# Kernel optimization log

Measured on AMD Instinct MI355X. Metric: run time of the kernel, lower is better.

## Reference

```python
import jax, jax.numpy as jnp
import numpy as np

INPUT_SIZE = 128
HID = 64
B, T = 256, 1024

def setup_inputs() -> dict:
    key = jax.random.key(0)
    ks = jax.random.split(key, 12)
    s1 = 1.0 / np.sqrt(HID)
    def u(k, shape):
        return jax.random.uniform(k, shape, jnp.float32, -s1, s1)
    return {
        "x": jax.random.normal(ks[0], (B, T, INPUT_SIZE), jnp.float32),
        "w_ih0": u(ks[1], (4 * HID, INPUT_SIZE)),
        "w_hh0": u(ks[2], (4 * HID, HID)),
        "b_ih0": u(ks[3], (4 * HID,)),
        "b_hh0": u(ks[4], (4 * HID,)),
        "w_ih1": u(ks[5], (4 * HID, HID)),
        "w_hh1": u(ks[6], (4 * HID, HID)),
        "b_ih1": u(ks[7], (4 * HID,)),
        "b_hh1": u(ks[8], (4 * HID,)),
        "w_out": u(ks[9], (1, HID)),
        "b_out": u(ks[10], (1,)),
    }

def _lstm(x, w_ih, w_hh, b_ih, b_hh):
    # x: [B, T, I] -> h sequence [B, T, H]; PyTorch gate order i, f, g, o
    Bb = x.shape[0]
    H = w_hh.shape[1]
    # precompute input contribution for all timesteps (one big GEMM)
    xg = jnp.einsum('bti,gi->btg', x, w_ih) + b_ih + b_hh  # [B, T, 4H]
    def step(carry, g_t):
        h, c = carry
        g = g_t + h @ w_hh.T  # [B, 4H]
        i, f, gg, o = jnp.split(g, 4, axis=-1)
        i = jax.nn.sigmoid(i)
        f = jax.nn.sigmoid(f)
        gg = jnp.tanh(gg)
        o = jax.nn.sigmoid(o)
        c = f * c + i * gg
        h = o * jnp.tanh(c)
        return (h, c), h
    init = (jnp.zeros((Bb, H), x.dtype), jnp.zeros((Bb, H), x.dtype))
    _, hs = jax.lax.scan(step, init, jnp.swapaxes(xg, 0, 1))  # [T, B, H]
    return jnp.swapaxes(hs, 0, 1)

def reference(x, w_ih0, w_hh0, b_ih0, b_hh0, w_ih1, w_hh1, b_ih1, b_hh1, w_out, b_out):
    h1 = _lstm(x, w_ih0, w_hh0, b_ih0, b_hh0)   # [B, T, H]
    h2 = _lstm(h1, w_ih1, w_hh1, b_ih1, b_hh1)  # [B, T, H]
    logits = jnp.einsum('bth,oh->bto', h2, w_out) + b_out  # [B, T, 1]
    return jax.nn.sigmoid(logits)
```

## Files before the change

### kernel.cpp

```cpp
#include <hip/hip_runtime.h>

#define BB 256
#define TT 1024
#define II 128
#define HH 64
#define BT (BB * TT)

typedef _Float16 h2 __attribute__((ext_vector_type(2)));
typedef _Float16 half8 __attribute__((ext_vector_type(8)));
typedef float f32x4 __attribute__((ext_vector_type(4)));
typedef unsigned int uint;
typedef unsigned short ushort;

#define DOT2(a, b, c) __builtin_amdgcn_fdot2((a), (b), (c), false)
#define BC(u) __builtin_bit_cast(h2, (uint)(u))
#define MFMA16(a, b, c) __builtin_amdgcn_mfma_f32_16x16x32_f16((a), (b), (c), 0, 0, 0)
#define SIG(v) __builtin_amdgcn_rcpf(1.0f + __expf(-(v)))
#define TNH(v) (1.0f - 2.0f * __builtin_amdgcn_rcpf(1.0f + __expf(2.0f * (v))))

#define BAR() asm volatile("s_waitcnt lgkmcnt(0)\n\ts_barrier" ::: "memory")

#define LDPK(P, ptr) uint P; { float2 _f = *(const float2*)(ptr); \
    h2 _h; _h[0] = (_Float16)_f.x; _h[1] = (_Float16)_f.y; \
    P = __builtin_bit_cast(uint, _h); }
#define PIN8(a,b,c,d,e,f,g,h_) asm volatile("" : "+v"(a),"+v"(b),"+v"(c),"+v"(d),"+v"(e),"+v"(f),"+v"(g),"+v"(h_));
#define LD8(P, base, o) \
    LDPK(P##0,(base)+(o)+ 0) LDPK(P##1,(base)+(o)+ 2) LDPK(P##2,(base)+(o)+ 4) LDPK(P##3,(base)+(o)+ 6) \
    LDPK(P##4,(base)+(o)+ 8) LDPK(P##5,(base)+(o)+10) LDPK(P##6,(base)+(o)+12) LDPK(P##7,(base)+(o)+14) \
    PIN8(P##0,P##1,P##2,P##3,P##4,P##5,P##6,P##7)

#define D8A(P, va, vb, c0, c1, c2, c3) \
    c0 = DOT2(BC(P##0), BC((va).x), c0); c1 = DOT2(BC(P##1), BC((va).y), c1); \
    c2 = DOT2(BC(P##2), BC((va).z), c2); c3 = DOT2(BC(P##3), BC((va).w), c3); \
    c0 = DOT2(BC(P##4), BC((vb).x), c0); c1 = DOT2(BC(P##5), BC((vb).y), c1); \
    c2 = DOT2(BC(P##6), BC((vb).z), c2); c3 = DOT2(BC(P##7), BC((vb).w), c3);

#define GDOT(G, s) { float a0=0.f,a1=0.f,a2=0.f,a3=0.f; \
    D8A(G##A, hv0, hv1, a0,a1,a2,a3) D8A(G##B, hv2, hv3, a0,a1,a2,a3) \
    D8A(G##C, hv4, hv5, a0,a1,a2,a3) D8A(G##D, hv6, hv7, a0,a1,a2,a3) \
    s = (a0 + a1) + (a2 + a3); }

__global__ __launch_bounds__(256)
void xg_mfma(const float* __restrict__ x, const float* __restrict__ w_ih0,
             ushort* __restrict__ xg)
{
    __shared__ __align__(16) _Float16 xt[64][136];
    __shared__ __align__(16) _Float16 wt[128][136];
    const int tid = threadIdx.x, lane = tid & 63, wv = tid >> 6;
    const int bt0 = blockIdx.x * 64;
    {
        const int row = tid >> 2, q = (tid & 3) * 32;
        const float4* src = (const float4*)(x + (size_t)(bt0 + row) * II + q);
        _Float16* dst = &xt[row][q];
        #pragma unroll
        for (int i = 0; i < 8; ++i) {
            float4 v = src[i];
            dst[4*i+0]=(_Float16)v.x; dst[4*i+1]=(_Float16)v.y;
            dst[4*i+2]=(_Float16)v.z; dst[4*i+3]=(_Float16)v.w;
        }
    }
    for (int nh = 0; nh < 2; ++nh) {
        __syncthreads();
        {
            const int n = tid >> 1, kh = (tid & 1) * 64;
            const float4* src = (const float4*)(w_ih0 + (size_t)(nh * 128 + n) * II + kh);
            _Float16* dst = &wt[n][kh];
            #pragma unroll
            for (int i = 0; i < 16; ++i) {
                float4 v = src[i];
                dst[4*i+0]=(_Float16)v.x; dst[4*i+1]=(_Float16)v.y;
                dst[4*i+2]=(_Float16)v.z; dst[4*i+3]=(_Float16)v.w;
            }
        }
        __syncthreads();
        const int m = wv * 16 + (lane & 15);
        const int kf = (lane >> 4) * 8;
        half8 a0 = *(const half8*)&xt[m][ 0 + kf];
        half8 a1 = *(const half8*)&xt[m][32 + kf];
        half8 a2 = *(const half8*)&xt[m][64 + kf];
        half8 a3 = *(const half8*)&xt[m][96 + kf];
        #pragma unroll
        for (int nt = 0; nt < 8; ++nt) {
            const int nloc = nt * 16 + (lane & 15);
            half8 b0 = *(const half8*)&wt[nloc][ 0 + kf];
            half8 b1 = *(const half8*)&wt[nloc][32 + kf];
            half8 b2 = *(const half8*)&wt[nloc][64 + kf];
            half8 b3 = *(const half8*)&wt[nloc][96 + kf];
            f32x4 acc = {0.f, 0.f, 0.f, 0.f};
            acc = MFMA16(a0, b0, acc); acc = MFMA16(a1, b1, acc);
            acc = MFMA16(a2, b2, acc); acc = MFMA16(a3, b3, acc);
            const int col = nh * 128 + nt * 16 + (lane & 15);
            const int idx = (col & 63) * 4 + (col >> 6);
            const int r0  = wv * 16 + (lane >> 4) * 4;
            #pragma unroll
            for (int r = 0; r < 4; ++r) {
                _Float16 hv = (_Float16)acc[r];
                xg[(size_t)(bt0 + r0 + r) * 256 + idx] = __builtin_bit_cast(ushort, hv);
            }
        }
    }
}

__global__ __launch_bounds__(192) __attribute__((amdgpu_waves_per_eu(1, 1)))
void lstm2_core(const float* __restrict__ w_hh0,
                const float* __restrict__ b_ih0, const float* __restrict__ b_hh0,
                const float* __restrict__ w_ih1, const float* __restrict__ w_hh1,
                const float* __restrict__ b_ih1, const float* __restrict__ b_hh1,
                const ushort* __restrict__ xg, ushort* __restrict__ h1g)
{
    const int bb = blockIdx.x;
    const int w  = threadIdx.x >> 6;
    const int j  = threadIdx.x & 63;

    __shared__ __align__(16) uint  h0buf[2][32];
    __shared__ __align__(16) uint  h1buf[2][32];
    __shared__ float zbuf[2][4][68];

    const float* Wsel = (w == 0) ? w_hh0 : (w == 1) ? w_ih1 : w_hh1;
    const float* r0p = Wsel + (size_t)(  0 + j) * 64;
    const float* r1p = Wsel + (size_t)( 64 + j) * 64;
    const float* r2p = Wsel + (size_t)(128 + j) * 64;
    const float* r3p = Wsel + (size_t)(192 + j) * 64;
    LD8(G0A, r0p,  0) LD8(G0B, r0p, 16) LD8(G0C, r0p, 32) LD8(G0D, r0p, 48)
    LD8(G1A, r1p,  0) LD8(G1B, r1p, 16) LD8(G1C, r1p, 32) LD8(G1D, r1p, 48)
    LD8(G2A, r2p,  0) LD8(G2B, r2p, 16) LD8(G2C, r2p, 32) LD8(G2D, r2p, 48)
    LD8(G3A, r3p,  0) LD8(G3B, r3p, 16) LD8(G3C, r3p, 32) LD8(G3D, r3p, 48)

    float bI = 0.f, bF = 0.f, bG = 0.f, bO = 0.f;
    if (w == 0) {
        bI = b_ih0[j]       + b_hh0[j];
        bF = b_ih0[64 + j]  + b_hh0[64 + j];
        bG = b_ih0[128 + j] + b_hh0[128 + j];
        bO = b_ih0[192 + j] + b_hh0[192 + j];
    } else if (w == 2) {
        bI = b_ih1[j]       + b_hh1[j];
        bF = b_ih1[64 + j]  + b_hh1[64 + j];
        bG = b_ih1[128 + j] + b_hh1[128 + j];
        bO = b_ih1[192 + j] + b_hh1[192 + j];
    }

    float cst = 0.0f;
    const ushort* xbase = xg + (size_t)bb * TT * 256 + j * 4;
    ushort* h1b = h1g + (size_t)bb * TT * 64 + j;

    if (threadIdx.x < 32)       h0buf[1][threadIdx.x] = 0u;
    else if (threadIdx.x < 64)  h1buf[1][threadIdx.x - 32] = 0u;
    __syncthreads();

    uint2 xc = {0,0}, xn1 = {0,0}, xn2 = {0,0};
    if (w == 0) {
        xc  = *(const uint2*)(xbase);
        xn1 = *(const uint2*)(xbase + 256);
    }

    for (int k = 0; k < TT + 2; ++k) {
        if (w == 0) {
            if (k + 2 < TT) xn2 = *(const uint2*)(xbase + (size_t)(k + 2) * 256);
            if (k < TT) {
                const uint4* hq = (const uint4*)&h0buf[(k + 1) & 1][0];
                uint4 hv0=hq[0], hv1=hq[1], hv2=hq[2], hv3=hq[3];
                uint4 hv4=hq[4], hv5=hq[5], hv6=hq[6], hv7=hq[7];
                float si, sf, sg, so;
                GDOT(G0, si) GDOT(G1, sf) GDOT(G2, sg) GDOT(G3, so)
                h2 xlo = BC(xc.x), xhi = BC(xc.y);
                si += bI + (float)xlo[0]; sf += bF + (float)xlo[1];
                sg += bG + (float)xhi[0]; so += bO + (float)xhi[1];
                float ii = SIG(si), ff = SIG(sf), gg = TNH(sg), oo = SIG(so);
                cst = fmaf(ff, cst, ii * gg);
                float hval = oo * TNH(cst);
                ((_Float16*)&h0buf[k & 1][0])[j] = (_Float16)hval;
            }
            xc = xn1; xn1 = xn2;
        } else if (w == 1) {
            if (k >= 1 && k <= TT) {
                const int m = k - 1;
                const uint4* hq = (const uint4*)&h0buf[m & 1][0];
                uint4 hv0=hq[0], hv1=hq[1], hv2=hq[2], hv3=hq[3];
                uint4 hv4=hq[4], hv5=hq[5], hv6=hq[6], hv7=hq[7];
                float si, sf, sg, so;
                GDOT(G0, si) GDOT(G1, sf) GDOT(G2, sg) GDOT(G3, so)
                const int s = m & 1;
                zbuf[s][0][j] = si; zbuf[s][1][j] = sf;
                zbuf[s][2][j] = sg; zbuf[s][3][j] = so;
            }
        } else {
            if (k >= 2) {
                const int m = k - 2;
                const int s = m & 1;
                const uint4* hq = (const uint4*)&h1buf[(m + 1) & 1][0];
                uint4 hv0=hq[0], hv1=hq[1], hv2=hq[2], hv3=hq[3];
                uint4 hv4=hq[4], hv5=hq[5], hv6=hq[6], hv7=hq[7];
                float si, sf, sg, so;
                GDOT(G0, si) GDOT(G1, sf) GDOT(G2, sg) GDOT(G3, so)
                si += bI + zbuf[s][0][j]; sf += bF + zbuf[s][1][j];
                sg += bG + zbuf[s][2][j]; so += bO + zbuf[s][3][j];
                float ii = SIG(si), ff = SIG(sf), gg = TNH(sg), oo = SIG(so);
                cst = fmaf(ff, cst, ii * gg);
                float hval = oo * TNH(cst);
                _Float16 hf = (_Float16)hval;
                ((_Float16*)&h1buf[m & 1][0])[j] = hf;
                h1b[(size_t)m * 64] = __builtin_bit_cast(ushort, hf);
            }
        }
        BAR();
    }
}

__global__ __launch_bounds__(256)
void head_gemv(const ushort* __restrict__ h1g, const float* __restrict__ w_out,
               const float* __restrict__ b_out, float* __restrict__ outp)
{
    __shared__ float wsh[64];
    const int tid = threadIdx.x;
    if (tid < 64) wsh[tid] = w_out[tid];
    __syncthreads();
    const int bt = blockIdx.x * 256 + tid;
    const uint4* hp = (const uint4*)(h1g + (size_t)bt * 64);
    float s = 0.0f;
    #pragma unroll
    for (int i = 0; i < 8; ++i) {
        uint4 v = hp[i];
        const float* wp = &wsh[8 * i];
        h2 p;
        p = BC(v.x); s = fmaf((float)p[0], wp[0], s); s = fmaf((float)p[1], wp[1], s);
        p = BC(v.y); s = fmaf((float)p[0], wp[2], s); s = fmaf((float)p[1], wp[3], s);
        p = BC(v.z); s = fmaf((float)p[0], wp[4], s); s = fmaf((float)p[1], wp[5], s);
        p = BC(v.w); s = fmaf((float)p[0], wp[6], s); s = fmaf((float)p[1], wp[7], s);
    }
    outp[bt] = __builtin_amdgcn_rcpf(1.0f + __expf(-(s + b_out[0])));
}

extern "C" void kernel_launch(void* const* d_in, const int* in_sizes, int n_in,
                              void* d_out, int out_size, void* d_ws, size_t ws_size,
                              hipStream_t stream) {
    const float* x     = (const float*)d_in[0];
    const float* w_ih0 = (const float*)d_in[1];
    const float* w_hh0 = (const float*)d_in[2];
    const float* b_ih0 = (const float*)d_in[3];
    const float* b_hh0 = (const float*)d_in[4];
    const float* w_ih1 = (const float*)d_in[5];
    const float* w_hh1 = (const float*)d_in[6];
    const float* b_ih1 = (const float*)d_in[7];
    const float* b_hh1 = (const float*)d_in[8];
    const float* w_out = (const float*)d_in[9];
    const float* b_out = (const float*)d_in[10];
    float* out = (float*)d_out;

    ushort* xg  = (ushort*)d_ws;
    ushort* h1g = (ushort*)((char*)d_ws + (size_t)BT * 256 * 2);

    hipLaunchKernelGGL(xg_mfma, dim3(BT / 64), dim3(256), 0, stream, x, w_ih0, xg);
    hipLaunchKernelGGL(lstm2_core, dim3(BB), dim3(192), 0, stream,
                       w_hh0, b_ih0, b_hh0, w_ih1, w_hh1, b_ih1, b_hh1, xg, h1g);
    hipLaunchKernelGGL(head_gemv, dim3(BT / 256), dim3(256), 0, stream,
                       h1g, w_out, b_out, out);
}
```

Baseline: 823.1 us.

## Split LSTM gate rows across two waves per role to halve serial dot chain

The recurrent kernel now uses six waves instead of three: each role (layer-0 recurrence, layer-1 input projection, layer-1 recurrence) is split over two waves, and each lane computes two gate rows instead of four. Gate activations are exchanged between lane halves with cross-lane shuffles. The xg layout is changed to plain gate-major columns to match. This shortens the per-timestep dependent dot-product chain at the cost of extra shuffles, scalar 16-bit global loads, and a six-wave barrier each step.

```diff
diff --git a/kernel.cpp b/kernel.cpp
--- a/kernel.cpp
+++ b/kernel.cpp
@@ -15,8 +15,7 @@
 #define DOT2(a, b, c) __builtin_amdgcn_fdot2((a), (b), (c), false)
 #define BC(u) __builtin_bit_cast(h2, (uint)(u))
 #define MFMA16(a, b, c) __builtin_amdgcn_mfma_f32_16x16x32_f16((a), (b), (c), 0, 0, 0)
-#define SIG(v) __builtin_amdgcn_rcpf(1.0f + __expf(-(v)))
-#define TNH(v) (1.0f - 2.0f * __builtin_amdgcn_rcpf(1.0f + __expf(2.0f * (v))))
+#define RCP(v) __builtin_amdgcn_rcpf(v)
 
 #define BAR() asm volatile("s_waitcnt lgkmcnt(0)\n\ts_barrier" ::: "memory")
 
@@ -35,10 +34,13 @@
     c0 = DOT2(BC(P##4), BC((vb).x), c0); c1 = DOT2(BC(P##5), BC((vb).y), c1); \
     c2 = DOT2(BC(P##6), BC((vb).z), c2); c3 = DOT2(BC(P##7), BC((vb).w), c3);
 
-#define GDOT(G, s) { float a0=0.f,a1=0.f,a2=0.f,a3=0.f; \
-    D8A(G##A, hv0, hv1, a0,a1,a2,a3) D8A(G##B, hv2, hv3, a0,a1,a2,a3) \
-    D8A(G##C, hv4, hv5, a0,a1,a2,a3) D8A(G##D, hv6, hv7, a0,a1,a2,a3) \
-    s = (a0 + a1) + (a2 + a3); }
+#define DUALDOT(sA, sB) { \
+    float a0=0.f,a1=0.f,a2=0.f,a3=0.f, b0=0.f,b1=0.f,b2=0.f,b3=0.f; \
+    D8A(A0, hv0, hv1, a0,a1,a2,a3) D8A(A1, hv2, hv3, a0,a1,a2,a3) \
+    D8A(A2, hv4, hv5, a0,a1,a2,a3) D8A(A3, hv6, hv7, a0,a1,a2,a3) \
+    D8A(B0, hv0, hv1, b0,b1,b2,b3) D8A(B1, hv2, hv3, b0,b1,b2,b3) \
+    D8A(B2, hv4, hv5, b0,b1,b2,b3) D8A(B3, hv6, hv7, b0,b1,b2,b3) \
+    sA = (a0 + a1) + (a2 + a3); sB = (b0 + b1) + (b2 + b3); }
 
 __global__ __launch_bounds__(256)
 void xg_mfma(const float* __restrict__ x, const float* __restrict__ w_ih0,
@@ -90,116 +92,128 @@
             acc = MFMA16(a0, b0, acc); acc = MFMA16(a1, b1, acc);
             acc = MFMA16(a2, b2, acc); acc = MFMA16(a3, b3, acc);
             const int col = nh * 128 + nt * 16 + (lane & 15);
-            const int idx = (col & 63) * 4 + (col >> 6);
             const int r0  = wv * 16 + (lane >> 4) * 4;
             #pragma unroll
             for (int r = 0; r < 4; ++r) {
                 _Float16 hv = (_Float16)acc[r];
-                xg[(size_t)(bt0 + r0 + r) * 256 + idx] = __builtin_bit_cast(ushort, hv);
-            }
-        }
-    }
-}
-
-__global__ __launch_bounds__(192) __attribute__((amdgpu_waves_per_eu(1, 1)))
+                xg[(size_t)(bt0 + r0 + r) * 256 + col] = __builtin_bit_cast(ushort, hv);
+            }
+        }
+    }
+}
+
+__global__ __launch_bounds__(384) __attribute__((amdgpu_waves_per_eu(1, 1)))
 void lstm2_core(const float* __restrict__ w_hh0,
                 const float* __restrict__ b_ih0, const float* __restrict__ b_hh0,
                 const float* __restrict__ w_ih1, const float* __restrict__ w_hh1,
                 const float* __restrict__ b_ih1, const float* __restrict__ b_hh1,
                 const ushort* __restrict__ xg, ushort* __restrict__ h1g)
 {
-    const int bb = blockIdx.x;
-    const int w  = threadIdx.x >> 6;
-    const int j  = threadIdx.x & 63;
-
-    __shared__ __align__(16) uint  h0buf[2][32];
-    __shared__ __align__(16) uint  h1buf[2][32];
+    const int bb   = blockIdx.x;
+    const int w    = threadIdx.x >> 6;
+    const int l    = threadIdx.x & 63;
+    const int role = w >> 1;
+    const int gp   = l >> 5;
+    const int j    = (w & 1) * 32 + (l & 31);
+    const int rA   = gp * 128 + j;
+    const int rB   = rA + 64;
+
+    __shared__ __align__(16) uint h0buf[2][32];
+    __shared__ __align__(16) uint h1buf[2][32];
     __shared__ float zbuf[2][4][68];
 
-    const float* Wsel = (w == 0) ? w_hh0 : (w == 1) ? w_ih1 : w_hh1;
-    const float* r0p = Wsel + (size_t)(  0 + j) * 64;
-    const float* r1p = Wsel + (size_t)( 64 + j) * 64;
-    const float* r2p = Wsel + (size_t)(128 + j) * 64;
-    const float* r3p = Wsel + (size_t)(192 + j) * 64;
-    LD8(G0A, r0p,  0) LD8(G0B, r0p, 16) LD8(G0C, r0p, 32) LD8(G0D, r0p, 48)
-    LD8(G1A, r1p,  0) LD8(G1B, r1p, 16) LD8(G1C, r1p, 32) LD8(G1D, r1p, 48)
-    LD8(G2A, r2p,  0) LD8(G2B, r2p, 16) LD8(G2C, r2p, 32) LD8(G2D, r2p, 48)
-    LD8(G3A, r3p,  0) LD8(G3B, r3p, 16) LD8(G3C, r3p, 32) LD8(G3D, r3p, 48)
-
-    float bI = 0.f, bF = 0.f, bG = 0.f, bO = 0.f;
-    if (w == 0) {
-        bI = b_ih0[j]       + b_hh0[j];
-        bF = b_ih0[64 + j]  + b_hh0[64 + j];
-        bG = b_ih0[128 + j] + b_hh0[128 + j];
-        bO = b_ih0[192 + j] + b_hh0[192 + j];
-    } else if (w == 2) {
-        bI = b_ih1[j]       + b_hh1[j];
-        bF = b_ih1[64 + j]  + b_hh1[64 + j];
-        bG = b_ih1[128 + j] + b_hh1[128 + j];
-        bO = b_ih1[192 + j] + b_hh1[192 + j];
-    }
+    const float* M = (role == 0) ? w_hh0 : (role == 1) ? w_ih1 : w_hh1;
+    const float* pA = M + (size_t)rA * 64;
+    const float* pB = M + (size_t)rB * 64;
+    LD8(A0, pA,  0) LD8(A1, pA, 16) LD8(A2, pA, 32) LD8(A3, pA, 48)
+    LD8(B0, pB,  0) LD8(B1, pB, 16) LD8(B2, pB, 32) LD8(B3, pB, 48)
+
+    float bA = 0.f, bB = 0.f;
+    if (role == 0)      { bA = b_ih0[rA] + b_hh0[rA]; bB = b_ih0[rB] + b_hh0[rB]; }
+    else if (role == 1) { bA = b_ih1[rA] + b_hh1[rA]; bB = b_ih1[rB] + b_hh1[rB]; }
+
+    const float nscA = gp ?  2.0f : -1.0f;
+    const float acoA = gp ?  1.0f :  0.0f;
+    const float bcoA = gp ? -1.0f :  1.0f;
 
     float cst = 0.0f;
-    const ushort* xbase = xg + (size_t)bb * TT * 256 + j * 4;
+    const ushort* xbA = xg + (size_t)bb * TT * 256 + rA;
+    const ushort* xbB = xg + (size_t)bb * TT * 256 + rB;
     ushort* h1b = h1g + (size_t)bb * TT * 64 + j;
 
-    if (threadIdx.x < 32)       h0buf[1][threadIdx.x] = 0u;
-    else if (threadIdx.x < 64)  h1buf[1][threadIdx.x - 32] = 0u;
+    if (threadIdx.x < 32)      h0buf[1][threadIdx.x] = 0u;
+    else if (threadIdx.x < 64) h1buf[1][threadIdx.x - 32] = 0u;
     __syncthreads();
 
-    uint2 xc = {0,0}, xn1 = {0,0}, xn2 = {0,0};
-    if (w == 0) {
-        xc  = *(const uint2*)(xbase);
-        xn1 = *(const uint2*)(xbase + 256);
+    ushort xcA = 0, xcB = 0, x1A = 0, x1B = 0, x2A = 0, x2B = 0;
+    if (role == 0) {
+        xcA = xbA[0];   xcB = xbB[0];
+        x1A = xbA[256]; x1B = xbB[256];
     }
 
     for (int k = 0; k < TT + 2; ++k) {
-        if (w == 0) {
-            if (k + 2 < TT) xn2 = *(const uint2*)(xbase + (size_t)(k + 2) * 256);
+        if (role == 0) {
+            if (k + 2 < TT) { x2A = xbA[(size_t)(k + 2) * 256];
+                              x2B = xbB[(size_t)(k + 2) * 256]; }
             if (k < TT) {
                 const uint4* hq = (const uint4*)&h0buf[(k + 1) & 1][0];
                 uint4 hv0=hq[0], hv1=hq[1], hv2=hq[2], hv3=hq[3];
                 uint4 hv4=hq[4], hv5=hq[5], hv6=hq[6], hv7=hq[7];
-                float si, sf, sg, so;
-                GDOT(G0, si) GDOT(G1, sf) GDOT(G2, sg) GDOT(G3, so)
-                h2 xlo = BC(xc.x), xhi = BC(xc.y);
-                si += bI + (float)xlo[0]; sf += bF + (float)xlo[1];
-                sg += bG + (float)xhi[0]; so += bO + (float)xhi[1];
-                float ii = SIG(si), ff = SIG(sf), gg = TNH(sg), oo = SIG(so);
+                float sA, sB;
+                DUALDOT(sA, sB)
+                sA += bA + (float)__builtin_bit_cast(_Float16, xcA);
+                sB += bB + (float)__builtin_bit_cast(_Float16, xcB);
+                float yA   = __expf(nscA * sA);
+                float actA = fmaf(acoA, yA, bcoA) * RCP(yA + 1.0f);
+                float actB = RCP(1.0f + __expf(-sB));
+                float oA = __shfl_xor(actA, 32, 64);
+                float oB = __shfl_xor(actB, 32, 64);
+                float ii = gp ? oA : actA;
+                float ff = gp ? oB : actB;
+                float gg = gp ? actA : oA;
+                float oo = gp ? actB : oB;
                 cst = fmaf(ff, cst, ii * gg);
-                float hval = oo * TNH(cst);
-                ((_Float16*)&h0buf[k & 1][0])[j] = (_Float16)hval;
-            }
-            xc = xn1; xn1 = xn2;
-        } else if (w == 1) {
+                float hval = oo * (1.0f - 2.0f * RCP(1.0f + __expf(2.0f * cst)));
+                if (gp == 0) ((_Float16*)&h0buf[k & 1][0])[j] = (_Float16)hval;
+            }
+            xcA = x1A; xcB = x1B; x1A = x2A; x1B = x2B;
+        } else if (role == 1) {
             if (k >= 1 && k <= TT) {
-                const int m = k - 1;
-                const uint4* hq = (const uint4*)&h0buf[m & 1][0];
+                const int m = k - 1, s = m & 1;
+                const uint4* hq = (const uint4*)&h0buf[s][0];
                 uint4 hv0=hq[0], hv1=hq[1], hv2=hq[2], hv3=hq[3];
                 uint4 hv4=hq[4], hv5=hq[5], hv6=hq[6], hv7=hq[7];
-                float si, sf, sg, so;
-                GDOT(G0, si) GDOT(G1, sf) GDOT(G2, sg) GDOT(G3, so)
-                const int s = m & 1;
-                zbuf[s][0][j] = si; zbuf[s][1][j] = sf;
-                zbuf[s][2][j] = sg; zbuf[s][3][j] = so;
+                float sA, sB;
+                DUALDOT(sA, sB)
+                zbuf[s][2 * gp][j]     = sA + bA;
+                zbuf[s][2 * gp + 1][j] = sB + bB;
             }
         } else {
             if (k >= 2) {
-                const int m = k - 2;
-                const int s = m & 1;
+                const int m = k - 2, s = m & 1;
                 const uint4* hq = (const uint4*)&h1buf[(m + 1) & 1][0];
                 uint4 hv0=hq[0], hv1=hq[1], hv2=hq[2], hv3=hq[3];
                 uint4 hv4=hq[4], hv5=hq[5], hv6=hq[6], hv7=hq[7];
-                float si, sf, sg, so;
-                GDOT(G0, si) GDOT(G1, sf) GDOT(G2, sg) GDOT(G3, so)
-                si += bI + zbuf[s][0][j]; sf += bF + zbuf[s][1][j];
-                sg += bG + zbuf[s][2][j]; so += bO + zbuf[s][3][j];
-                float ii = SIG(si), ff = SIG(sf), gg = TNH(sg), oo = SIG(so);
+                float sA, sB;
+                DUALDOT(sA, sB)
+                sA += zbuf[s][2 * gp][j];
+                sB += zbuf[s][2 * gp + 1][j];
+                float yA   = __expf(nscA * sA);
+                float actA = fmaf(acoA, yA, bcoA) * RCP(yA + 1.0f);
+                float actB = RCP(1.0f + __expf(-sB));
+                float oA = __shfl_xor(actA, 32, 64);
+                float oB = __shfl_xor(actB, 32, 64);
+                float ii = gp ? oA : actA;
+                float ff = gp ? oB : actB;
+                float gg = gp ? actA : oA;
+                float oo = gp ? actB : oB;
                 cst = fmaf(ff, cst, ii * gg);
-                float hval = oo * TNH(cst);
-                _Float16 hf = (_Float16)hval;
-                ((_Float16*)&h1buf[m & 1][0])[j] = hf;
-                h1b[(size_t)m * 64] = __builtin_bit_cast(ushort, hf);
+                float hval = oo * (1.0f - 2.0f * RCP(1.0f + __expf(2.0f * cst)));
+                if (gp == 0) {
+                    _Float16 hf = (_Float16)hval;
+                    ((_Float16*)&h1buf[s][0])[j] = hf;
+                    h1b[(size_t)m * 64] = __builtin_bit_cast(ushort, hf);
+                }
             }
         }
         BAR();
@@ -227,7 +241,7 @@
         p = BC(v.z); s = fmaf((float)p[0], wp[4], s); s = fmaf((float)p[1], wp[5], s);
         p = BC(v.w); s = fmaf((float)p[0], wp[6], s); s = fmaf((float)p[1], wp[7], s);
     }
-    outp[bt] = __builtin_amdgcn_rcpf(1.0f + __expf(-(s + b_out[0])));
+    outp[bt] = RCP(1.0f + __expf(-(s + b_out[0])));
 }
 
 extern "C" void kernel_launch(void* const* d_in, const int* in_sizes, int n_in,
@@ -250,7 +264,7 @@
     ushort* h1g = (ushort*)((char*)d_ws + (size_t)BT * 256 * 2);
 
     hipLaunchKernelGGL(xg_mfma, dim3(BT / 64), dim3(256), 0, stream, x, w_ih0, xg);
-    hipLaunchKernelGGL(lstm2_core, dim3(BB), dim3(192), 0, stream,
+    hipLaunchKernelGGL(lstm2_core, dim3(BB), dim3(384), 0, stream,
                        w_hh0, b_ih0, b_hh0, w_ih1, w_hh1, b_ih1, b_hh1, xg, h1g);
     hipLaunchKernelGGL(head_gemv, dim3(BT / 256), dim3(256), 0, stream,
                        h1g, w_out, b_out, out);
```

Measured after the change: 884.7 us. +7.5%, slower.

## Keep full W_ih0 resident per block and unroll recurrence loop by two

Applied to the files above, without the earlier changes.

The input-projection kernel now loads all 256 rows of w_ih0 into shared memory once and loops over four 64-row x tiles, so each block covers 256 timesteps and the weight reload and conversion are amortised. The recurrent kernel is manually unrolled by two with compile-time buffer parity, replacing the three-deep x prefetch rotation with two alternating registers. This removes per-step index arithmetic and register moves on the serial critical path. The trade-off is larger shared memory per projection block and fewer blocks for the projection.

```diff
diff --git a/kernel.cpp b/kernel.cpp
--- a/kernel.cpp
+++ b/kernel.cpp
@@ -44,43 +44,47 @@
 void xg_mfma(const float* __restrict__ x, const float* __restrict__ w_ih0,
              ushort* __restrict__ xg)
 {
+    __shared__ __align__(16) _Float16 wt[256][136];
     __shared__ __align__(16) _Float16 xt[64][136];
-    __shared__ __align__(16) _Float16 wt[128][136];
     const int tid = threadIdx.x, lane = tid & 63, wv = tid >> 6;
-    const int bt0 = blockIdx.x * 64;
-    {
-        const int row = tid >> 2, q = (tid & 3) * 32;
-        const float4* src = (const float4*)(x + (size_t)(bt0 + row) * II + q);
-        _Float16* dst = &xt[row][q];
+    const int bt0 = blockIdx.x * 256;
+
+    #pragma unroll
+    for (int p = 0; p < 2; ++p) {
+        const int n = p * 128 + (tid >> 1), kh = (tid & 1) * 64;
+        const float4* src = (const float4*)(w_ih0 + (size_t)n * II + kh);
+        _Float16* dst = &wt[n][kh];
         #pragma unroll
-        for (int i = 0; i < 8; ++i) {
+        for (int i = 0; i < 16; ++i) {
             float4 v = src[i];
             dst[4*i+0]=(_Float16)v.x; dst[4*i+1]=(_Float16)v.y;
             dst[4*i+2]=(_Float16)v.z; dst[4*i+3]=(_Float16)v.w;
         }
     }
-    for (int nh = 0; nh < 2; ++nh) {
+
+    for (int grp = 0; grp < 4; ++grp) {
         __syncthreads();
         {
-            const int n = tid >> 1, kh = (tid & 1) * 64;
-            const float4* src = (const float4*)(w_ih0 + (size_t)(nh * 128 + n) * II + kh);
-            _Float16* dst = &wt[n][kh];
+            const int row = tid >> 2, q = (tid & 3) * 32;
+            const float4* src = (const float4*)(x + (size_t)(bt0 + grp * 64 + row) * II + q);
+            _Float16* dst = &xt[row][q];
             #pragma unroll
-            for (int i = 0; i < 16; ++i) {
+            for (int i = 0; i < 8; ++i) {
                 float4 v = src[i];
                 dst[4*i+0]=(_Float16)v.x; dst[4*i+1]=(_Float16)v.y;
                 dst[4*i+2]=(_Float16)v.z; dst[4*i+3]=(_Float16)v.w;
             }
         }
         __syncthreads();
-        const int m = wv * 16 + (lane & 15);
+
+        const int m  = wv * 16 + (lane & 15);
         const int kf = (lane >> 4) * 8;
         half8 a0 = *(const half8*)&xt[m][ 0 + kf];
         half8 a1 = *(const half8*)&xt[m][32 + kf];
         half8 a2 = *(const half8*)&xt[m][64 + kf];
         half8 a3 = *(const half8*)&xt[m][96 + kf];
         #pragma unroll
-        for (int nt = 0; nt < 8; ++nt) {
+        for (int nt = 0; nt < 16; ++nt) {
             const int nloc = nt * 16 + (lane & 15);
             half8 b0 = *(const half8*)&wt[nloc][ 0 + kf];
             half8 b1 = *(const half8*)&wt[nloc][32 + kf];
@@ -89,9 +93,9 @@
             f32x4 acc = {0.f, 0.f, 0.f, 0.f};
             acc = MFMA16(a0, b0, acc); acc = MFMA16(a1, b1, acc);
             acc = MFMA16(a2, b2, acc); acc = MFMA16(a3, b3, acc);
-            const int col = nh * 128 + nt * 16 + (lane & 15);
+            const int col = nt * 16 + (lane & 15);
             const int idx = (col & 63) * 4 + (col >> 6);
-            const int r0  = wv * 16 + (lane >> 4) * 4;
+            const int r0  = grp * 64 + wv * 16 + (lane >> 4) * 4;
             #pragma unroll
             for (int r = 0; r < 4; ++r) {
                 _Float16 hv = (_Float16)acc[r];
@@ -100,6 +104,50 @@
         }
     }
 }
+
+#define STEP(K_, E_, XC_) { \
+    if (w == 0) { \
+        if ((K_) < TT) { \
+            const uint4* hq = (const uint4*)&h0buf[1-(E_)][0]; \
+            uint4 hv0=hq[0], hv1=hq[1], hv2=hq[2], hv3=hq[3]; \
+            uint4 hv4=hq[4], hv5=hq[5], hv6=hq[6], hv7=hq[7]; \
+            float si, sf, sg, so; \
+            GDOT(G0, si) GDOT(G1, sf) GDOT(G2, sg) GDOT(G3, so) \
+            h2 xlo = BC((XC_).x), xhi = BC((XC_).y); \
+            si += bI + (float)xlo[0]; sf += bF + (float)xlo[1]; \
+            sg += bG + (float)xhi[0]; so += bO + (float)xhi[1]; \
+            float ii = SIG(si), ff = SIG(sf), gg = TNH(sg), oo = SIG(so); \
+            cst = fmaf(ff, cst, ii * gg); \
+            float hval = oo * TNH(cst); \
+            ((_Float16*)&h0buf[(E_)][0])[j] = (_Float16)hval; \
+        } \
+    } else if (w == 1) { \
+        if ((K_) >= 1 && (K_) <= TT) { \
+            const uint4* hq = (const uint4*)&h0buf[1-(E_)][0]; \
+            uint4 hv0=hq[0], hv1=hq[1], hv2=hq[2], hv3=hq[3]; \
+            uint4 hv4=hq[4], hv5=hq[5], hv6=hq[6], hv7=hq[7]; \
+            float si, sf, sg, so; \
+            GDOT(G0, si) GDOT(G1, sf) GDOT(G2, sg) GDOT(G3, so) \
+            zbuf[1-(E_)][0][j] = si; zbuf[1-(E_)][1][j] = sf; \
+            zbuf[1-(E_)][2][j] = sg; zbuf[1-(E_)][3][j] = so; \
+        } \
+    } else { \
+        if ((K_) >= 2) { \
+            const uint4* hq = (const uint4*)&h1buf[1-(E_)][0]; \
+            uint4 hv0=hq[0], hv1=hq[1], hv2=hq[2], hv3=hq[3]; \
+            uint4 hv4=hq[4], hv5=hq[5], hv6=hq[6], hv7=hq[7]; \
+            float si, sf, sg, so; \
+            GDOT(G0, si) GDOT(G1, sf) GDOT(G2, sg) GDOT(G3, so) \
+            si += bI + zbuf[(E_)][0][j]; sf += bF + zbuf[(E_)][1][j]; \
+            sg += bG + zbuf[(E_)][2][j]; so += bO + zbuf[(E_)][3][j]; \
+            float ii = SIG(si), ff = SIG(sf), gg = TNH(sg), oo = SIG(so); \
+            cst = fmaf(ff, cst, ii * gg); \
+            float hval = oo * TNH(cst); \
+            _Float16 hf = (_Float16)hval; \
+            ((_Float16*)&h1buf[(E_)][0])[j] = hf; \
+            h1b[(size_t)((K_) - 2) * 64] = __builtin_bit_cast(ushort, hf); \
+        } \
+    } }
 
 __global__ __launch_bounds__(192) __attribute__((amdgpu_waves_per_eu(1, 1)))
 void lstm2_core(const float* __restrict__ w_hh0,
@@ -147,61 +195,20 @@
     else if (threadIdx.x < 64)  h1buf[1][threadIdx.x - 32] = 0u;
     __syncthreads();
 
-    uint2 xc = {0,0}, xn1 = {0,0}, xn2 = {0,0};
+    uint2 xA = {0,0}, xB = {0,0};
     if (w == 0) {
-        xc  = *(const uint2*)(xbase);
-        xn1 = *(const uint2*)(xbase + 256);
-    }
-
-    for (int k = 0; k < TT + 2; ++k) {
-        if (w == 0) {
-            if (k + 2 < TT) xn2 = *(const uint2*)(xbase + (size_t)(k + 2) * 256);
-            if (k < TT) {
-                const uint4* hq = (const uint4*)&h0buf[(k + 1) & 1][0];
-                uint4 hv0=hq[0], hv1=hq[1], hv2=hq[2], hv3=hq[3];
-                uint4 hv4=hq[4], hv5=hq[5], hv6=hq[6], hv7=hq[7];
-                float si, sf, sg, so;
-                GDOT(G0, si) GDOT(G1, sf) GDOT(G2, sg) GDOT(G3, so)
-                h2 xlo = BC(xc.x), xhi = BC(xc.y);
-                si += bI + (float)xlo[0]; sf += bF + (float)xlo[1];
-                sg += bG + (float)xhi[0]; so += bO + (float)xhi[1];
-                float ii = SIG(si), ff = SIG(sf), gg = TNH(sg), oo = SIG(so);
-                cst = fmaf(ff, cst, ii * gg);
-                float hval = oo * TNH(cst);
-                ((_Float16*)&h0buf[k & 1][0])[j] = (_Float16)hval;
-            }
-            xc = xn1; xn1 = xn2;
-        } else if (w == 1) {
-            if (k >= 1 && k <= TT) {
-                const int m = k - 1;
-                const uint4* hq = (const uint4*)&h0buf[m & 1][0];
-                uint4 hv0=hq[0], hv1=hq[1], hv2=hq[2], hv3=hq[3];
-                uint4 hv4=hq[4], hv5=hq[5], hv6=hq[6], hv7=hq[7];
-                float si, sf, sg, so;
-                GDOT(G0, si) GDOT(G1, sf) GDOT(G2, sg) GDOT(G3, so)
-                const int s = m & 1;
-                zbuf[s][0][j] = si; zbuf[s][1][j] = sf;
-                zbuf[s][2][j] = sg; zbuf[s][3][j] = so;
-            }
-        } else {
-            if (k >= 2) {
-                const int m = k - 2;
-                const int s = m & 1;
-                const uint4* hq = (const uint4*)&h1buf[(m + 1) & 1][0];
-                uint4 hv0=hq[0], hv1=hq[1], hv2=hq[2], hv3=hq[3];
-                uint4 hv4=hq[4], hv5=hq[5], hv6=hq[6], hv7=hq[7];
-                float si, sf, sg, so;
-                GDOT(G0, si) GDOT(G1, sf) GDOT(G2, sg) GDOT(G3, so)
-                si += bI + zbuf[s][0][j]; sf += bF + zbuf[s][1][j];
-                sg += bG + zbuf[s][2][j]; so += bO + zbuf[s][3][j];
-                float ii = SIG(si), ff = SIG(sf), gg = TNH(sg), oo = SIG(so);
-                cst = fmaf(ff, cst, ii * gg);
-                float hval = oo * TNH(cst);
-                _Float16 hf = (_Float16)hval;
-                ((_Float16*)&h1buf[m & 1][0])[j] = hf;
-                h1b[(size_t)m * 64] = __builtin_bit_cast(ushort, hf);
-            }
-        }
+        xA = *(const uint2*)(xbase);
+        xB = *(const uint2*)(xbase + 256);
+    }
+
+    for (int kk = 0; kk <= TT; kk += 2) {
+        STEP(kk, 0, xA)
+        if (w == 0 && kk + 2 < TT)
+            xA = *(const uint2*)(xbase + (size_t)(kk + 2) * 256);
+        BAR();
+        STEP(kk + 1, 1, xB)
+        if (w == 0 && kk + 3 < TT)
+            xB = *(const uint2*)(xbase + (size_t)(kk + 3) * 256);
         BAR();
     }
 }
@@ -249,7 +256,7 @@
     ushort* xg  = (ushort*)d_ws;
     ushort* h1g = (ushort*)((char*)d_ws + (size_t)BT * 256 * 2);
 
-    hipLaunchKernelGGL(xg_mfma, dim3(BT / 64), dim3(256), 0, stream, x, w_ih0, xg);
+    hipLaunchKernelGGL(xg_mfma, dim3(BT / 256), dim3(256), 0, stream, x, w_ih0, xg);
     hipLaunchKernelGGL(lstm2_core, dim3(BB), dim3(192), 0, stream,
                        w_hh0, b_ih0, b_hh0, w_ih1, w_hh1, b_ih1, b_hh1, xg, h1g);
     hipLaunchKernelGGL(head_gemv, dim3(BT / 256), dim3(256), 0, stream,
```

Measured after the change: 823.7 us. Within noise of the previous version (+0.1%).
